# Kernel optimization log

Hardware: AMD Instinct MI355X
Metric: run time of the kernel (lower is better)

## Reference

```python
import jax, jax.numpy as jnp
import numpy as np

N_HEAD = 12

def setup_inputs() -> dict:
    key = jax.random.key(0)
    ks = jax.random.split(key, 5)
    B, T, C = 4, 2048, 768
    x = jax.random.normal(ks[0], (B, T, C), dtype=jnp.float32)
    s_in = 1.0 / np.sqrt(C)
    W_qkv = jax.random.normal(ks[1], (C, 3 * C), dtype=jnp.float32) * s_in
    b_qkv = jnp.zeros((3 * C,), dtype=jnp.float32)
    W_proj = jax.random.normal(ks[2], (C, C), dtype=jnp.float32) * s_in
    b_proj = jnp.zeros((C,), dtype=jnp.float32)
    return {"x": x, "W_qkv": W_qkv, "b_qkv": b_qkv, "W_proj": W_proj, "b_proj": b_proj}


def reference(x, W_qkv, b_qkv, W_proj, b_proj):
    B, T, C = x.shape
    H = N_HEAD
    D = C // H  # head dim
    qkv = x @ W_qkv + b_qkv                      # [B,T,3C]
    q, k, v = jnp.split(qkv, 3, axis=-1)
    # [B,T,C] -> [B,H,T,D]
    q = q.reshape(B, T, H, D).transpose(0, 2, 1, 3)
    k = k.reshape(B, T, H, D).transpose(0, 2, 1, 3)
    v = v.reshape(B, T, H, D).transpose(0, 2, 1, 3)
    att = jnp.einsum("bhqd,bhkd->bhqk", q, k) / jnp.sqrt(jnp.asarray(D, x.dtype))
    causal = jnp.tril(jnp.ones((T, T), dtype=bool))
    att = jnp.where(causal, att, jnp.asarray(-jnp.inf, att.dtype))
    att = jax.nn.softmax(att, axis=-1)
    y = jnp.einsum("bhqk,bhkd->bhqd", att, v)    # [B,H,T,D]
    y = y.transpose(0, 2, 1, 3).reshape(B, T, C)
    return y @ W_proj + b_proj
```

## Files before the change

kernel.cpp:

```cpp
#include <hip/hip_runtime.h>
#include <hip/hip_bf16.h>

typedef __bf16 bf16x8 __attribute__((ext_vector_type(8)));
typedef float f32x4 __attribute__((ext_vector_type(4)));
typedef unsigned int u32x4 __attribute__((ext_vector_type(4)));
typedef unsigned int u32x2 __attribute__((ext_vector_type(2)));
typedef unsigned short u16;
typedef unsigned long long u64;

__device__ __forceinline__ u16 f2bf(float f) {
  unsigned u = __builtin_bit_cast(unsigned, f);
  u += 0x7FFFu + ((u >> 16) & 1u);
  return (u16)(u >> 16);
}
__device__ __forceinline__ unsigned cvtpk(float a, float b) {
  float2 f; f.x = a; f.y = b;
  __hip_bfloat162 h = __float22bfloat162_rn(f);
  unsigned u;
  __builtin_memcpy(&u, &h, 4);
  return u;
}

__device__ __forceinline__ void gll16(const u16* g, u16* l) {
  __builtin_amdgcn_global_load_lds(
      (const __attribute__((address_space(1))) unsigned int*)g,
      (__attribute__((address_space(3))) unsigned int*)l, 16, 0, 0);
}

__global__ void cast_x_kernel(const float* __restrict__ in, u16* __restrict__ out, int n4) {
  int i = blockIdx.x * blockDim.x + threadIdx.x;
  if (i >= n4) return;
  f32x4 v = *(const f32x4*)(in + (size_t)i * 4);
  u32x2 pk;
  pk[0] = cvtpk(v[0], v[1]);
  pk[1] = cvtpk(v[2], v[3]);
  *(u32x2*)(out + (size_t)i * 4) = pk;
}

__global__ void transpose_cast_kernel(const float* __restrict__ W, u16* __restrict__ WT, int K, int N) {
  __shared__ float tile[32][33];
  int c0 = blockIdx.x * 32, r0 = blockIdx.y * 32;
  int tx = threadIdx.x & 31, tg = threadIdx.x >> 5;
#pragma unroll
  for (int i = 0; i < 4; ++i) {
    int r = tg + i * 8;
    tile[r][tx] = W[(size_t)(r0 + r) * N + c0 + tx];
  }
  __syncthreads();
#pragma unroll
  for (int i = 0; i < 4; ++i) {
    int r = tg + i * 8;
    WT[(size_t)(c0 + r) * K + r0 + tx] = f2bf(tile[tx][r]);
  }
}

#define GEMM128_MAINLOOP(A, BT, m0, n0)                                                     \
  constexpr int K = 768;                                                                    \
  __shared__ u16 Asm[128 * 32];                                                             \
  __shared__ u16 Bsm[128 * 32];                                                             \
  const int tid = threadIdx.x;                                                              \
  const int w = tid >> 6, lane = tid & 63;                                                  \
  const int l15 = lane & 15, quad = lane >> 4;                                              \
  const int srow = tid >> 2, scol = (tid & 3) * 8;                                          \
  const u16* Ag0 = (A) + (size_t)((m0) + srow) * K + scol;                                  \
  const u16* Ag1 = (A) + (size_t)((m0) + 64 + srow) * K + scol;                             \
  const u16* Bg0 = (BT) + (size_t)((n0) + srow) * K + scol;                                 \
  const u16* Bg1 = (BT) + (size_t)((n0) + 64 + srow) * K + scol;                            \
  u16* Al0 = &Asm[(w * 64) * 8];                                                            \
  u16* Al1 = &Asm[(256 + w * 64) * 8];                                                      \
  u16* Bl0 = &Bsm[(w * 64) * 8];                                                            \
  u16* Bl1 = &Bsm[(256 + w * 64) * 8];                                                      \
  const int mw = (w >> 1) * 64, nw = (w & 1) * 64;                                          \
  f32x4 acc[4][4];                                                                          \
  _Pragma("unroll") for (int i = 0; i < 4; ++i) _Pragma("unroll") for (int j = 0; j < 4;    \
                                                                       ++j) acc[i][j] = {   \
      0.f, 0.f, 0.f, 0.f};                                                                  \
  for (int k0 = 0; k0 < K; k0 += 32) {                                                      \
    __syncthreads();                                                                        \
    gll16(Ag0 + k0, Al0);                                                                   \
    gll16(Ag1 + k0, Al1);                                                                   \
    gll16(Bg0 + k0, Bl0);                                                                   \
    gll16(Bg1 + k0, Bl1);                                                                   \
    __syncthreads();                                                                        \
    bf16x8 af[4], bfj[4];                                                                   \
    _Pragma("unroll") for (int i = 0; i < 4; ++i) af[i] =                                   \
        *(const bf16x8*)&Asm[(mw + i * 16 + l15) * 32 + quad * 8];                          \
    _Pragma("unroll") for (int j = 0; j < 4; ++j) bfj[j] =                                  \
        *(const bf16x8*)&Bsm[(nw + j * 16 + l15) * 32 + quad * 8];                          \
    _Pragma("unroll") for (int i = 0; i < 4; ++i) _Pragma("unroll") for (int j = 0; j < 4;  \
                                                                         ++j) acc[i][j] =  \
        __builtin_amdgcn_mfma_f32_16x16x32_bf16(af[i], bfj[j], acc[i][j], 0, 0, 0);         \
  }

__global__ __launch_bounds__(256) void gemm_qkv_kernel(
    const u16* __restrict__ A, const u16* __restrict__ BT, const float* __restrict__ bias,
    u16* __restrict__ Qb, u16* __restrict__ Kb, u16* __restrict__ Vt) {
  const int m0 = blockIdx.y * 128, n0 = blockIdx.x * 128;
  GEMM128_MAINLOOP(A, BT, m0, n0)
  const int sec = blockIdx.x / 6;
  const int nbase = n0 - sec * 768;
#pragma unroll
  for (int j = 0; j < 4; ++j) {
    const int nloc = nbase + nw + j * 16 + l15;
    const float bv = bias[sec * 768 + nloc];
    const int h = nloc >> 6, d = nloc & 63;
#pragma unroll
    for (int i = 0; i < 4; ++i) {
      const int m = m0 + mw + i * 16 + quad * 4;
      const int bb = m >> 11, trow = m & 2047;
      if (sec == 2) {
        u32x2 pk;
        pk[0] = cvtpk(acc[i][j][0] + bv, acc[i][j][1] + bv);
        pk[1] = cvtpk(acc[i][j][2] + bv, acc[i][j][3] + bv);
        *(u32x2*)(Vt + (size_t)((bb * 12 + h) * 64 + d) * 2048 + trow) = pk;
      } else {
        u16* dst = (sec == 0) ? Qb : Kb;
        const float scl = (sec == 0) ? 0.125f * 1.44269504f : 1.0f;
#pragma unroll
        for (int r = 0; r < 4; ++r)
          dst[(size_t)((bb * 12 + h) * 2048 + trow + r) * 64 + d] = f2bf((acc[i][j][r] + bv) * scl);
      }
    }
  }
}

__global__ __launch_bounds__(256) void gemm_proj_kernel(
    const u16* __restrict__ A, const u16* __restrict__ BT, const float* __restrict__ bias,
    float* __restrict__ out) {
  const int m0 = blockIdx.y * 128, n0 = blockIdx.x * 128;
  GEMM128_MAINLOOP(A, BT, m0, n0)
#pragma unroll
  for (int j = 0; j < 4; ++j) {
    const int n = n0 + nw + j * 16 + l15;
    const float bv = bias[n];
#pragma unroll
    for (int i = 0; i < 4; ++i) {
      const int m = m0 + mw + i * 16 + quad * 4;
#pragma unroll
      for (int r = 0; r < 4; ++r) out[(size_t)(m + r) * 768 + n] = acc[i][j][r] + bv;
    }
  }
}

__global__ __launch_bounds__(256) void attn_kernel(
    const u16* __restrict__ Qg, const u16* __restrict__ Kg, const u16* __restrict__ Vtg,
    u16* __restrict__ Yb) {
  constexpr int T = 2048, D = 64;
  constexpr int LDP = 72;
  constexpr float MBOUND = 20.0f;
  __shared__ u16 Ks[64 * LDP];
  __shared__ u16 VTs[64 * LDP];
  __shared__ u16 Ps[4 * 32 * LDP];
  const int qb = 15 - blockIdx.x;
  const int bh = blockIdx.y;
  const int Q0 = qb * 128;
  const int bidx = bh / 12, hidx = bh % 12;
  const int tid = threadIdx.x;
  const int w = tid >> 6, lane = tid & 63;
  const int l15 = lane & 15, quad = lane >> 4;
  const int srow = tid >> 2, scol = (tid & 3) * 16;
  const u16* Kp = Kg + (size_t)bh * T * D;
  const u16* VTp = Vtg + (size_t)bh * D * T;
  u16* pw0 = &Ps[(w * 32) * LDP];
  u16* pw1 = &Ps[(w * 32 + 16) * LDP];

  const u16* qrow0 = Qg + ((size_t)bh * T + Q0 + w * 16 + l15) * D;
  const bf16x8 qf0a = *(const bf16x8*)(qrow0 + quad * 8);
  const bf16x8 qf0b = *(const bf16x8*)(qrow0 + 32 + quad * 8);
  const bf16x8 qf1a = *(const bf16x8*)(qrow0 + (size_t)64 * D + quad * 8);
  const bf16x8 qf1b = *(const bf16x8*)(qrow0 + (size_t)64 * D + 32 + quad * 8);
  const int qq0 = Q0 + w * 16 + l15, qq1 = qq0 + 64;

  f32x4 o0[4] = {{0,0,0,0},{0,0,0,0},{0,0,0,0},{0,0,0,0}};
  f32x4 o1[4] = {{0,0,0,0},{0,0,0,0},{0,0,0,0},{0,0,0,0}};
  float l0v = 0.f, l1v = 0.f;

  const int nkt = 2 * qb + 2;
  u32x4 kA = *(const u32x4*)(Kp + (size_t)srow * D + scol);
  u32x4 kB = *(const u32x4*)(Kp + (size_t)srow * D + scol + 8);
  u32x4 vA = *(const u32x4*)(VTp + (size_t)srow * T + scol);
  u32x4 vB = *(const u32x4*)(VTp + (size_t)srow * T + scol + 8);

  for (int kt = 0; kt < nkt; ++kt) {
    __syncthreads();
    *(u32x4*)&Ks[srow * LDP + scol] = kA;
    *(u32x4*)&Ks[srow * LDP + scol + 8] = kB;
    *(u32x4*)&VTs[srow * LDP + scol] = vA;
    *(u32x4*)&VTs[srow * LDP + scol + 8] = vB;
    __syncthreads();
    if (kt + 1 < nkt) {
      const int k1 = (kt + 1) * 64;
      kA = *(const u32x4*)(Kp + (size_t)(k1 + srow) * D + scol);
      kB = *(const u32x4*)(Kp + (size_t)(k1 + srow) * D + scol + 8);
      vA = *(const u32x4*)(VTp + (size_t)srow * T + k1 + scol);
      vB = *(const u32x4*)(VTp + (size_t)srow * T + k1 + scol + 8);
    }
    const int k0 = kt * 64;
    const bool g0a = (kt <= 2 * qb);

    f32x4 s0[4] = {{0,0,0,0},{0,0,0,0},{0,0,0,0},{0,0,0,0}};
    f32x4 s1[4] = {{0,0,0,0},{0,0,0,0},{0,0,0,0},{0,0,0,0}};
#pragma unroll
    for (int t = 0; t < 4; ++t) {
      const bf16x8 kf0 = *(const bf16x8*)&Ks[(t * 16 + l15) * LDP + quad * 8];
      const bf16x8 kf1 = *(const bf16x8*)&Ks[(t * 16 + l15) * LDP + 32 + quad * 8];
      s0[t] = __builtin_amdgcn_mfma_f32_16x16x32_bf16(kf0, qf0a, s0[t], 0, 0, 0);
      s0[t] = __builtin_amdgcn_mfma_f32_16x16x32_bf16(kf1, qf0b, s0[t], 0, 0, 0);
      s1[t] = __builtin_amdgcn_mfma_f32_16x16x32_bf16(kf0, qf1a, s1[t], 0, 0, 0);
      s1[t] = __builtin_amdgcn_mfma_f32_16x16x32_bf16(kf1, qf1b, s1[t], 0, 0, 0);
    }
    if (g0a) {
      if (kt == 2 * qb) {
#pragma unroll
        for (int t = 0; t < 4; ++t)
#pragma unroll
          for (int r = 0; r < 4; ++r)
            if (k0 + t * 16 + quad * 4 + r > qq0) s0[t][r] = -1e30f;
      }
#pragma unroll
      for (int t = 0; t < 4; ++t) {
        float e0 = __builtin_amdgcn_exp2f(s0[t][0] - MBOUND);
        float e1 = __builtin_amdgcn_exp2f(s0[t][1] - MBOUND);
        float e2 = __builtin_amdgcn_exp2f(s0[t][2] - MBOUND);
        float e3 = __builtin_amdgcn_exp2f(s0[t][3] - MBOUND);
        l0v += (e0 + e1) + (e2 + e3);
        u32x2 pk;
        pk[0] = cvtpk(e0, e1);
        pk[1] = cvtpk(e2, e3);
        *(u32x2*)&pw0[l15 * LDP + t * 16 + quad * 4] = pk;
      }
    }
    {
      if (kt == 2 * qb + 1) {
#pragma unroll
        for (int t = 0; t < 4; ++t)
#pragma unroll
          for (int r = 0; r < 4; ++r)
            if (k0 + t * 16 + quad * 4 + r > qq1) s1[t][r] = -1e30f;
      }
#pragma unroll
      for (int t = 0; t < 4; ++t) {
        float e0 = __builtin_amdgcn_exp2f(s1[t][0] - MBOUND);
        float e1 = __builtin_amdgcn_exp2f(s1[t][1] - MBOUND);
        float e2 = __builtin_amdgcn_exp2f(s1[t][2] - MBOUND);
        float e3 = __builtin_amdgcn_exp2f(s1[t][3] - MBOUND);
        l1v += (e0 + e1) + (e2 + e3);
        u32x2 pk;
        pk[0] = cvtpk(e0, e1);
        pk[1] = cvtpk(e2, e3);
        *(u32x2*)&pw1[l15 * LDP + t * 16 + quad * 4] = pk;
      }
    }
    const bf16x8 p0a = *(const bf16x8*)&pw0[l15 * LDP + quad * 8];
    const bf16x8 p0b = *(const bf16x8*)&pw0[l15 * LDP + 32 + quad * 8];
    const bf16x8 p1a = *(const bf16x8*)&pw1[l15 * LDP + quad * 8];
    const bf16x8 p1b = *(const bf16x8*)&pw1[l15 * LDP + 32 + quad * 8];
#pragma unroll
    for (int t = 0; t < 4; ++t) {
      const bf16x8 vf0 = *(const bf16x8*)&VTs[(t * 16 + l15) * LDP + quad * 8];
      const bf16x8 vf1 = *(const bf16x8*)&VTs[(t * 16 + l15) * LDP + 32 + quad * 8];
      if (g0a) {
        o0[t] = __builtin_amdgcn_mfma_f32_16x16x32_bf16(vf0, p0a, o0[t], 0, 0, 0);
        o0[t] = __builtin_amdgcn_mfma_f32_16x16x32_bf16(vf1, p0b, o0[t], 0, 0, 0);
      }
      o1[t] = __builtin_amdgcn_mfma_f32_16x16x32_bf16(vf0, p1a, o1[t], 0, 0, 0);
      o1[t] = __builtin_amdgcn_mfma_f32_16x16x32_bf16(vf1, p1b, o1[t], 0, 0, 0);
    }
  }
  l0v += __shfl_xor(l0v, 16); l0v += __shfl_xor(l0v, 32);
  l1v += __shfl_xor(l1v, 16); l1v += __shfl_xor(l1v, 32);
  const float inv0 = 1.f / l0v, inv1 = 1.f / l1v;
  u16* y0 = Yb + ((size_t)bidx * T + qq0) * 768 + hidx * 64;
  u16* y1 = Yb + ((size_t)bidx * T + qq1) * 768 + hidx * 64;
#pragma unroll
  for (int t = 0; t < 4; ++t) {
    u32x2 pk0, pk1;
    pk0[0] = cvtpk(o0[t][0] * inv0, o0[t][1] * inv0);
    pk0[1] = cvtpk(o0[t][2] * inv0, o0[t][3] * inv0);
    pk1[0] = cvtpk(o1[t][0] * inv1, o1[t][1] * inv1);
    pk1[1] = cvtpk(o1[t][2] * inv1, o1[t][3] * inv1);
    *(u32x2*)(y0 + t * 16 + quad * 4) = pk0;
    *(u32x2*)(y1 + t * 16 + quad * 4) = pk1;
  }
}

extern "C" void kernel_launch(void* const* d_in, const int* in_sizes, int n_in,
                              void* d_out, int out_size, void* d_ws, size_t ws_size,
                              hipStream_t stream) {
  const float* x = (const float*)d_in[0];
  const float* W_qkv = (const float*)d_in[1];
  const float* b_qkv = (const float*)d_in[2];
  const float* W_proj = (const float*)d_in[3];
  const float* b_proj = (const float*)d_in[4];
  float* out = (float*)d_out;

  constexpr size_t MC = (size_t)8192 * 768;
  u16* xb = (u16*)d_ws;
  u16* Qb = xb + MC;
  u16* Kb = Qb + MC;
  u16* Vt = Kb + MC;
  u16* Yb = Vt + MC;
  u16* WqkvT = Yb + MC;
  u16* WprojT = WqkvT + (size_t)2304 * 768;

  cast_x_kernel<<<6291456 / (4 * 256), 256, 0, stream>>>(x, xb, 6291456 / 4);
  transpose_cast_kernel<<<dim3(2304 / 32, 768 / 32), 256, 0, stream>>>(W_qkv, WqkvT, 768, 2304);
  transpose_cast_kernel<<<dim3(768 / 32, 768 / 32), 256, 0, stream>>>(W_proj, WprojT, 768, 768);
  gemm_qkv_kernel<<<dim3(18, 64), 256, 0, stream>>>(xb, WqkvT, b_qkv, Qb, Kb, Vt);
  attn_kernel<<<dim3(16, 48), 256, 0, stream>>>(Qb, Kb, Vt, Yb);
  gemm_proj_kernel<<<dim3(6, 64), 256, 0, stream>>>(Yb, WprojT, b_proj, out);
}
```

Baseline: 262.0 us.

## Split causal attention into key-chunks with a combine pass; shrink proj GEMM tile

Attention is rewritten as a split-K (flash-decoding style) kernel. Each block handles a 64-row query tile over up to 8 key tiles. Longer query rows are split into 2-4 chunks whose partial outputs and row sums go to fp32 workspace, and a separate combine kernel sums and normalizes them. This balances the triangular causal workload across 3840 blocks instead of 768 uneven ones. The cost is extra workspace traffic and one more launch. The projection GEMM also moves to a 64x128 tile to double the block count. The split path runs only if the workspace is large enough.

```diff
diff --git a/kernel.cpp b/kernel.cpp
--- a/kernel.cpp
+++ b/kernel.cpp
@@ -127,19 +127,202 @@
 __global__ __launch_bounds__(256) void gemm_proj_kernel(
     const u16* __restrict__ A, const u16* __restrict__ BT, const float* __restrict__ bias,
     float* __restrict__ out) {
-  const int m0 = blockIdx.y * 128, n0 = blockIdx.x * 128;
-  GEMM128_MAINLOOP(A, BT, m0, n0)
+  constexpr int K = 768;
+  __shared__ u16 Asm[64 * 32];
+  __shared__ u16 Bsm[128 * 32];
+  const int tid = threadIdx.x;
+  const int w = tid >> 6, lane = tid & 63;
+  const int l15 = lane & 15, quad = lane >> 4;
+  const int srow = tid >> 2, scol = (tid & 3) * 8;
+  const int m0 = blockIdx.y * 64, n0 = blockIdx.x * 128;
+  const u16* Ag = A + (size_t)(m0 + srow) * K + scol;
+  const u16* Bg0 = BT + (size_t)(n0 + srow) * K + scol;
+  const u16* Bg1 = BT + (size_t)(n0 + 64 + srow) * K + scol;
+  u16* Al = &Asm[(w * 64) * 8];
+  u16* Bl0 = &Bsm[(w * 64) * 8];
+  u16* Bl1 = &Bsm[(256 + w * 64) * 8];
+  const int mw = (w >> 1) * 32, nw = (w & 1) * 64;
+  f32x4 acc[2][4];
+#pragma unroll
+  for (int i = 0; i < 2; ++i)
+#pragma unroll
+    for (int j = 0; j < 4; ++j) acc[i][j] = {0.f, 0.f, 0.f, 0.f};
+  for (int k0 = 0; k0 < K; k0 += 32) {
+    __syncthreads();
+    gll16(Ag + k0, Al);
+    gll16(Bg0 + k0, Bl0);
+    gll16(Bg1 + k0, Bl1);
+    __syncthreads();
+    bf16x8 af[2], bfj[4];
+#pragma unroll
+    for (int i = 0; i < 2; ++i) af[i] = *(const bf16x8*)&Asm[(mw + i * 16 + l15) * 32 + quad * 8];
+#pragma unroll
+    for (int j = 0; j < 4; ++j) bfj[j] = *(const bf16x8*)&Bsm[(nw + j * 16 + l15) * 32 + quad * 8];
+#pragma unroll
+    for (int i = 0; i < 2; ++i)
+#pragma unroll
+      for (int j = 0; j < 4; ++j)
+        acc[i][j] = __builtin_amdgcn_mfma_f32_16x16x32_bf16(af[i], bfj[j], acc[i][j], 0, 0, 0);
+  }
 #pragma unroll
   for (int j = 0; j < 4; ++j) {
     const int n = n0 + nw + j * 16 + l15;
     const float bv = bias[n];
 #pragma unroll
-    for (int i = 0; i < 4; ++i) {
+    for (int i = 0; i < 2; ++i) {
       const int m = m0 + mw + i * 16 + quad * 4;
 #pragma unroll
       for (int r = 0; r < 4; ++r) out[(size_t)(m + r) * 768 + n] = acc[i][j][r] + bv;
     }
   }
+}
+
+__global__ __launch_bounds__(256) void attn_split_kernel(
+    const u16* __restrict__ Qg, const u16* __restrict__ Kg, const u16* __restrict__ Vtg,
+    u16* __restrict__ Yb, float* __restrict__ Opart, float* __restrict__ lpart) {
+  constexpr int T = 2048, D = 64;
+  constexpr int LDP = 72;
+  constexpr float MBOUND = 20.0f;
+  __shared__ u16 Ks[64 * LDP];
+  __shared__ u16 VTs[64 * LDP];
+  __shared__ u16 Ps[4 * 16 * LDP];
+  const int s = 79 - blockIdx.x;
+  const int bh = blockIdx.y;
+  int qt, c;
+  if (s < 8) { qt = s; c = 0; }
+  else if (s < 24) { qt = 8 + ((s - 8) >> 1); c = (s - 8) & 1; }
+  else if (s < 48) { int u = s - 24; int q3 = u / 3; qt = 16 + q3; c = u - 3 * q3; }
+  else { int u = s - 48; qt = 24 + (u >> 2); c = u & 3; }
+  const int niter = min(8, qt + 1 - 8 * c);
+  const int tid = threadIdx.x;
+  const int w = tid >> 6, lane = tid & 63;
+  const int l15 = lane & 15, quad = lane >> 4;
+  const int srow = tid >> 2, scol = (tid & 3) * 16;
+  const u16* Kp = Kg + (size_t)bh * T * D;
+  const u16* VTp = Vtg + (size_t)bh * D * T;
+  u16* pw = &Ps[(w * 16) * LDP];
+
+  const int qq = qt * 64 + w * 16 + l15;
+  const u16* qrow = Qg + ((size_t)bh * T + qq) * D;
+  const bf16x8 qfa = *(const bf16x8*)(qrow + quad * 8);
+  const bf16x8 qfb = *(const bf16x8*)(qrow + 32 + quad * 8);
+
+  f32x4 o[4] = {{0,0,0,0},{0,0,0,0},{0,0,0,0},{0,0,0,0}};
+  float lv = 0.f;
+
+  int ktg = c * 8;
+  u32x4 kA = *(const u32x4*)(Kp + (size_t)(ktg * 64 + srow) * D + scol);
+  u32x4 kB = *(const u32x4*)(Kp + (size_t)(ktg * 64 + srow) * D + scol + 8);
+  u32x4 vA = *(const u32x4*)(VTp + (size_t)srow * T + ktg * 64 + scol);
+  u32x4 vB = *(const u32x4*)(VTp + (size_t)srow * T + ktg * 64 + scol + 8);
+
+  for (int j = 0; j < niter; ++j) {
+    ktg = c * 8 + j;
+    __syncthreads();
+    *(u32x4*)&Ks[srow * LDP + scol] = kA;
+    *(u32x4*)&Ks[srow * LDP + scol + 8] = kB;
+    *(u32x4*)&VTs[srow * LDP + scol] = vA;
+    *(u32x4*)&VTs[srow * LDP + scol + 8] = vB;
+    __syncthreads();
+    if (j + 1 < niter) {
+      const int k1 = (ktg + 1) * 64;
+      kA = *(const u32x4*)(Kp + (size_t)(k1 + srow) * D + scol);
+      kB = *(const u32x4*)(Kp + (size_t)(k1 + srow) * D + scol + 8);
+      vA = *(const u32x4*)(VTp + (size_t)srow * T + k1 + scol);
+      vB = *(const u32x4*)(VTp + (size_t)srow * T + k1 + scol + 8);
+    }
+    f32x4 sA[4] = {{0,0,0,0},{0,0,0,0},{0,0,0,0},{0,0,0,0}};
+#pragma unroll
+    for (int t = 0; t < 4; ++t) {
+      const bf16x8 kf0 = *(const bf16x8*)&Ks[(t * 16 + l15) * LDP + quad * 8];
+      const bf16x8 kf1 = *(const bf16x8*)&Ks[(t * 16 + l15) * LDP + 32 + quad * 8];
+      sA[t] = __builtin_amdgcn_mfma_f32_16x16x32_bf16(kf0, qfa, sA[t], 0, 0, 0);
+      sA[t] = __builtin_amdgcn_mfma_f32_16x16x32_bf16(kf1, qfb, sA[t], 0, 0, 0);
+    }
+    if (ktg == qt) {
+      const int k0 = ktg * 64;
+#pragma unroll
+      for (int t = 0; t < 4; ++t)
+#pragma unroll
+        for (int r = 0; r < 4; ++r)
+          if (k0 + t * 16 + quad * 4 + r > qq) sA[t][r] = -1e30f;
+    }
+#pragma unroll
+    for (int t = 0; t < 4; ++t) {
+      float e0 = __builtin_amdgcn_exp2f(sA[t][0] - MBOUND);
+      float e1 = __builtin_amdgcn_exp2f(sA[t][1] - MBOUND);
+      float e2 = __builtin_amdgcn_exp2f(sA[t][2] - MBOUND);
+      float e3 = __builtin_amdgcn_exp2f(sA[t][3] - MBOUND);
+      lv += (e0 + e1) + (e2 + e3);
+      u32x2 pk;
+      pk[0] = cvtpk(e0, e1);
+      pk[1] = cvtpk(e2, e3);
+      *(u32x2*)&pw[l15 * LDP + t * 16 + quad * 4] = pk;
+    }
+    const bf16x8 pa = *(const bf16x8*)&pw[l15 * LDP + quad * 8];
+    const bf16x8 pb = *(const bf16x8*)&pw[l15 * LDP + 32 + quad * 8];
+#pragma unroll
+    for (int t = 0; t < 4; ++t) {
+      const bf16x8 vf0 = *(const bf16x8*)&VTs[(t * 16 + l15) * LDP + quad * 8];
+      const bf16x8 vf1 = *(const bf16x8*)&VTs[(t * 16 + l15) * LDP + 32 + quad * 8];
+      o[t] = __builtin_amdgcn_mfma_f32_16x16x32_bf16(vf0, pa, o[t], 0, 0, 0);
+      o[t] = __builtin_amdgcn_mfma_f32_16x16x32_bf16(vf1, pb, o[t], 0, 0, 0);
+    }
+  }
+  lv += __shfl_xor(lv, 16);
+  lv += __shfl_xor(lv, 32);
+  if (qt <= 7) {
+    const float inv = 1.f / lv;
+    const int bidx = bh / 12, hidx = bh % 12;
+    u16* y = Yb + ((size_t)bidx * T + qq) * 768 + hidx * 64;
+#pragma unroll
+    for (int t = 0; t < 4; ++t) {
+      u32x2 pk;
+      pk[0] = cvtpk(o[t][0] * inv, o[t][1] * inv);
+      pk[1] = cvtpk(o[t][2] * inv, o[t][3] * inv);
+      *(u32x2*)(y + t * 16 + quad * 4) = pk;
+    }
+  } else {
+    const size_t pidx = (size_t)bh * 80 + s;
+    float* Op = Opart + pidx * 4096 + (size_t)(w * 16 + l15) * 64;
+#pragma unroll
+    for (int t = 0; t < 4; ++t) *(f32x4*)(Op + t * 16 + quad * 4) = o[t];
+    if (quad == 0) lpart[pidx * 64 + w * 16 + l15] = lv;
+  }
+}
+
+__global__ __launch_bounds__(256) void attn_combine_kernel(
+    const float* __restrict__ Opart, const float* __restrict__ lpart, u16* __restrict__ Yb) {
+  constexpr int T = 2048;
+  const int qt = 8 + blockIdx.x;
+  const int bh = blockIdx.y;
+  const int nch = (qt < 16) ? 2 : (qt < 24) ? 3 : 4;
+  const int off = (qt < 16) ? 8 + (qt - 8) * 2 : (qt < 24) ? 24 + (qt - 16) * 3 : 48 + (qt - 24) * 4;
+  const size_t base = (size_t)bh * 80 + off;
+  const int tid = threadIdx.x;
+  const int q = tid >> 2, db = (tid & 3) * 16;
+  f32x4 o[4] = {{0,0,0,0},{0,0,0,0},{0,0,0,0},{0,0,0,0}};
+  float l = 0.f;
+  for (int cc = 0; cc < nch; ++cc) {
+    const float* Op = Opart + (base + cc) * 4096 + (size_t)q * 64 + db;
+#pragma unroll
+    for (int v = 0; v < 4; ++v) o[v] += *(const f32x4*)(Op + v * 4);
+    l += lpart[(base + cc) * 64 + q];
+  }
+  const float inv = 1.f / l;
+  const int bidx = bh / 12, hidx = bh % 12;
+  u16* y = Yb + ((size_t)bidx * T + qt * 64 + q) * 768 + hidx * 64 + db;
+  u32x4 pk;
+  pk[0] = cvtpk(o[0][0] * inv, o[0][1] * inv);
+  pk[1] = cvtpk(o[0][2] * inv, o[0][3] * inv);
+  pk[2] = cvtpk(o[1][0] * inv, o[1][1] * inv);
+  pk[3] = cvtpk(o[1][2] * inv, o[1][3] * inv);
+  *(u32x4*)y = pk;
+  pk[0] = cvtpk(o[2][0] * inv, o[2][1] * inv);
+  pk[1] = cvtpk(o[2][2] * inv, o[2][3] * inv);
+  pk[2] = cvtpk(o[3][0] * inv, o[3][1] * inv);
+  pk[3] = cvtpk(o[3][2] * inv, o[3][3] * inv);
+  *(u32x4*)(y + 8) = pk;
 }
 
 __global__ __launch_bounds__(256) void attn_kernel(
@@ -163,24 +346,20 @@
   const u16* VTp = Vtg + (size_t)bh * D * T;
   u16* pw0 = &Ps[(w * 32) * LDP];
   u16* pw1 = &Ps[(w * 32 + 16) * LDP];
-
   const u16* qrow0 = Qg + ((size_t)bh * T + Q0 + w * 16 + l15) * D;
   const bf16x8 qf0a = *(const bf16x8*)(qrow0 + quad * 8);
   const bf16x8 qf0b = *(const bf16x8*)(qrow0 + 32 + quad * 8);
   const bf16x8 qf1a = *(const bf16x8*)(qrow0 + (size_t)64 * D + quad * 8);
   const bf16x8 qf1b = *(const bf16x8*)(qrow0 + (size_t)64 * D + 32 + quad * 8);
   const int qq0 = Q0 + w * 16 + l15, qq1 = qq0 + 64;
-
   f32x4 o0[4] = {{0,0,0,0},{0,0,0,0},{0,0,0,0},{0,0,0,0}};
   f32x4 o1[4] = {{0,0,0,0},{0,0,0,0},{0,0,0,0},{0,0,0,0}};
   float l0v = 0.f, l1v = 0.f;
-
   const int nkt = 2 * qb + 2;
   u32x4 kA = *(const u32x4*)(Kp + (size_t)srow * D + scol);
   u32x4 kB = *(const u32x4*)(Kp + (size_t)srow * D + scol + 8);
   u32x4 vA = *(const u32x4*)(VTp + (size_t)srow * T + scol);
   u32x4 vB = *(const u32x4*)(VTp + (size_t)srow * T + scol + 8);
-
   for (int kt = 0; kt < nkt; ++kt) {
     __syncthreads();
     *(u32x4*)&Ks[srow * LDP + scol] = kA;
@@ -197,7 +376,6 @@
     }
     const int k0 = kt * 64;
     const bool g0a = (kt <= 2 * qb);
-
     f32x4 s0[4] = {{0,0,0,0},{0,0,0,0},{0,0,0,0},{0,0,0,0}};
     f32x4 s1[4] = {{0,0,0,0},{0,0,0,0},{0,0,0,0},{0,0,0,0}};
 #pragma unroll
@@ -302,11 +480,21 @@
   u16* Yb = Vt + MC;
   u16* WqkvT = Yb + MC;
   u16* WprojT = WqkvT + (size_t)2304 * 768;
+  constexpr size_t BASE_U16 = 5 * MC + (size_t)2304 * 768 + (size_t)768 * 768;
+  float* Opart = (float*)((u16*)d_ws + BASE_U16);
+  float* lpart = Opart + (size_t)3840 * 4096;
+  constexpr size_t NEED = BASE_U16 * 2 + ((size_t)3840 * 4096 + (size_t)3840 * 64) * 4;
+  const bool use_split = (ws_size >= NEED);
 
   cast_x_kernel<<<6291456 / (4 * 256), 256, 0, stream>>>(x, xb, 6291456 / 4);
   transpose_cast_kernel<<<dim3(2304 / 32, 768 / 32), 256, 0, stream>>>(W_qkv, WqkvT, 768, 2304);
   transpose_cast_kernel<<<dim3(768 / 32, 768 / 32), 256, 0, stream>>>(W_proj, WprojT, 768, 768);
   gemm_qkv_kernel<<<dim3(18, 64), 256, 0, stream>>>(xb, WqkvT, b_qkv, Qb, Kb, Vt);
-  attn_kernel<<<dim3(16, 48), 256, 0, stream>>>(Qb, Kb, Vt, Yb);
-  gemm_proj_kernel<<<dim3(6, 64), 256, 0, stream>>>(Yb, WprojT, b_proj, out);
-}
+  if (use_split) {
+    attn_split_kernel<<<dim3(80, 48), 256, 0, stream>>>(Qb, Kb, Vt, Yb, Opart, lpart);
+    attn_combine_kernel<<<dim3(24, 48), 256, 0, stream>>>(Opart, lpart, Yb);
+  } else {
+    attn_kernel<<<dim3(16, 48), 256, 0, stream>>>(Qb, Kb, Vt, Yb);
+  }
+  gemm_proj_kernel<<<dim3(6, 128), 256, 0, stream>>>(Yb, WprojT, b_proj, out);
+}
```

New measurement: 244.9 us. 1.07x faster.
